# Kernel optimization log

Hardware: AMD Instinct MI355X
Metric: run time of the kernel (lower is better)

Reference implementation:

```python
import jax, jax.numpy as jnp
import numpy as np

B, T, D, H = 4, 1024, 1024, 16


def setup_inputs() -> dict:
    key = jax.random.key(0)
    ks = jax.random.split(key, 7)
    x = jax.random.normal(ks[0], (B, T, D), dtype=jnp.float32)
    scale = 0.02
    Wq = jax.random.normal(ks[1], (D, D), dtype=jnp.float32) * scale
    Wk = jax.random.normal(ks[2], (D, D), dtype=jnp.float32) * scale
    Wv = jax.random.normal(ks[3], (D, D), dtype=jnp.float32) * scale
    bq = jax.random.normal(ks[4], (D,), dtype=jnp.float32) * scale
    bk = jax.random.normal(ks[5], (D,), dtype=jnp.float32) * scale
    bv = jax.random.normal(ks[6], (D,), dtype=jnp.float32) * scale
    temperature = jnp.ones((H, 1, 1), dtype=jnp.float32)  # nn.Parameter(torch.ones(H,1,1))
    return {"x": x, "Wq": Wq, "bq": bq, "Wk": Wk, "bk": bk, "Wv": Wv, "bv": bv,
            "temperature": temperature}


def reference(x, Wq, bq, Wk, bk, Wv, bv, temperature):
    b, t, d = x.shape
    h = temperature.shape[0]
    dh = d // h
    # torch: self.q(x).view(B, H, -1, T)  -- a RAW reshape of (B,T,D) -> (B,H,Dh,T)
    q = (x @ Wq + bq).reshape(b, h, dh, t)
    k = (x @ Wk + bk).reshape(b, h, dh, t)
    v = (x @ Wv + bv).reshape(b, h, dh, t)
    # attn = k^T @ v : (B,H,T,T), scaled per-head by temperature, softmax over last dim
    attn = jnp.einsum('bhdt,bhds->bhts', k, v) * temperature
    attn = jax.nn.softmax(attn, axis=-1)
    # out = q @ attn : (B,H,Dh,T), then RAW reshape back to (B,T,D)
    out = jnp.einsum('bhdt,bhts->bhds', q, attn)
    return out.reshape(b, t, d)
```

## Files before the change

### kernel.cpp

```cpp
#include <hip/hip_runtime.h>
#include <math.h>

#define Bv 4
#define Tv 1024
#define Dv 1024
#define Hv 16
#define DHv 64
#define L2E 1.4426950408889634f

typedef __attribute__((ext_vector_type(8))) short short8;
typedef __attribute__((ext_vector_type(4))) short short4v;
typedef __attribute__((ext_vector_type(4))) float f32x4;
typedef __attribute__((ext_vector_type(2))) int int2v;

#define MFMA16(a, b, c) __builtin_amdgcn_mfma_f32_16x16x32_bf16((a), (b), (c), 0, 0, 0)

__device__ __forceinline__ short f2bf(float f) {
    union { float f; unsigned u; } v; v.f = f;
    unsigned r = v.u + 0x7FFFu + ((v.u >> 16) & 1u);
    return (short)(r >> 16);
}

__device__ __forceinline__ float exp2_hw(float x) {
#if __has_builtin(__builtin_amdgcn_exp2f)
    return __builtin_amdgcn_exp2f(x);
#else
    return exp2f(x);
#endif
}
__device__ __forceinline__ float log2_hw(float x) {
#if __has_builtin(__builtin_amdgcn_logf)
    return __builtin_amdgcn_logf(x);
#else
    return log2f(x);
#endif
}

__device__ __forceinline__ int cvt_pk_bf16(float lo, float hi) {
    int r; asm("v_cvt_pk_bf16_f32 %0, %1, %2" : "=v"(r) : "v"(lo), "v"(hi)); return r;
}

__device__ __forceinline__ void async16(const void* g, void* l) {
    __builtin_amdgcn_global_load_lds(
        (const __attribute__((address_space(1))) void*)g,
        (__attribute__((address_space(3))) void*)l, 16, 0, 0);
}

__device__ __forceinline__ short8 frag64(const short* buf, int r, int cw) {
    return *(const short8*)&buf[r * 64 + ((cw ^ (r & 7)) << 3)];
}

__device__ __forceinline__ short8 frag32(const short* buf, int r, int cw) {
    return *(const short8*)&buf[r * 32 + (((cw ^ (r >> 1)) & 3) << 3)];
}

__global__ __launch_bounds__(256) void cast_x(const float* __restrict__ x, short* __restrict__ xp) {
    const int idx = blockIdx.x * 256 + threadIdx.x;
    const int t = idx >> 7, j = idx & 127;
    const float* src = x + (size_t)t * 1024 + j * 8;
    float4 f0 = ((const float4*)src)[0], f1 = ((const float4*)src)[1];
    short8 o;
    o[0] = f2bf(f0.x); o[1] = f2bf(f0.y); o[2] = f2bf(f0.z); o[3] = f2bf(f0.w);
    o[4] = f2bf(f1.x); o[5] = f2bf(f1.y); o[6] = f2bf(f1.z); o[7] = f2bf(f1.w);
    *(short8*)&xp[(j >> 2) * 131072 + t * 32 + (j & 3) * 8] = o;
}

__global__ __launch_bounds__(256) void w_cast_t(
    const float* __restrict__ Wq, const float* __restrict__ Wk, const float* __restrict__ Wv,
    short* __restrict__ Wt)
{
    const float* W = (blockIdx.z == 0) ? Wq : (blockIdx.z == 1) ? Wk : Wv;
    short* Wto = Wt + (size_t)blockIdx.z * 1048576;
    __shared__ short Tl[64 * 72];
    const int k0 = blockIdx.y * 64, n0 = blockIdx.x * 64;
    const int tid = threadIdx.x;
    {
        const int r = tid >> 2, c16 = (tid & 3) * 16;
        const float* src = W + (size_t)(k0 + r) * Dv + n0 + c16;
        float4 f0 = ((const float4*)src)[0], f1 = ((const float4*)src)[1];
        float4 f2 = ((const float4*)src)[2], f3 = ((const float4*)src)[3];
        short8 s0, s1;
        s0[0] = f2bf(f0.x); s0[1] = f2bf(f0.y); s0[2] = f2bf(f0.z); s0[3] = f2bf(f0.w);
        s0[4] = f2bf(f1.x); s0[5] = f2bf(f1.y); s0[6] = f2bf(f1.z); s0[7] = f2bf(f1.w);
        s1[0] = f2bf(f2.x); s1[1] = f2bf(f2.y); s1[2] = f2bf(f2.z); s1[3] = f2bf(f2.w);
        s1[4] = f2bf(f3.x); s1[5] = f2bf(f3.y); s1[6] = f2bf(f3.z); s1[7] = f2bf(f3.w);
        *(short8*)&Tl[r * 72 + c16] = s0;
        *(short8*)&Tl[r * 72 + c16 + 8] = s1;
    }
    __syncthreads();
#pragma unroll
    for (int p = 0; p < 2; p++) {
        const int n = p * 32 + (tid >> 3), j8 = (tid & 7) * 8;
        short8 o;
#pragma unroll
        for (int jj = 0; jj < 8; jj++) o[jj] = Tl[(j8 + jj) * 72 + n];
        const int kk = k0 + j8;
        *(short8*)&Wto[(kk >> 5) * 32768 + (size_t)(n0 + n) * 32 + (kk & 31)] = o;
    }
}

__global__ __launch_bounds__(256, 2) void qkv_mfma(
    const short* __restrict__ xp, const short* __restrict__ Wp,
    const float* __restrict__ bq, const float* __restrict__ bk, const float* __restrict__ bv,
    const float* __restrict__ temp,
    short* __restrict__ Qo, short* __restrict__ Kt, short* __restrict__ Vt)
{
    __shared__ short smem[30720];

    const int tid = threadIdx.x;
    const int lane = tid & 63, w = tid >> 6;
    const int q = lane >> 4, c = lane & 15;
    const int wr = w >> 1, wc = w & 1;
    const int L = blockIdx.x + 16 * blockIdx.y;
    const int n0 = (L >> 5) * 64;
    const int tm0 = (L & 31) * 128;

    int aOff[2];
#pragma unroll
    for (int p = 0; p < 2; p++) {
        const int idx = p * 256 + tid;
        const int r = idx >> 2, cs = idx & 3, cg = (cs ^ (r >> 1)) & 3;
        aOff[p] = (tm0 + r) * 32 + cg * 8;
    }
    const int br = tid >> 2, bcs = tid & 3, bcg = (bcs ^ (br >> 1)) & 3;
    const int bOff = (n0 + br) * 32 + bcg * 8;

    f32x4 acc[3][4][2] = {};

    auto stage = [&](int s, int kb) {
        short* base = smem + s * 10240;
#pragma unroll
        for (int p = 0; p < 2; p++)
            async16(xp + kb * 131072 + aOff[p], base + (p * 256 + tid) * 8);
#pragma unroll
        for (int z = 0; z < 3; z++)
            async16(Wp + z * 1048576 + kb * 32768 + bOff,
                    base + 4096 + z * 2048 + tid * 8);
    };
    auto compute = [&](int s) {
        const short* base = smem + s * 10240;
        short8 af[4];
#pragma unroll
        for (int m = 0; m < 4; m++) af[m] = frag32(base, wr * 64 + m * 16 + c, q);
        __builtin_amdgcn_s_setprio(1);
#pragma unroll
        for (int z = 0; z < 3; z++) {
            const short* Bz = base + 4096 + z * 2048;
            short8 b0 = frag32(Bz, wc * 32 + c, q);
            short8 b1 = frag32(Bz, wc * 32 + 16 + c, q);
#pragma unroll
            for (int m = 0; m < 4; m++) {
                acc[z][m][0] = MFMA16(af[m], b0, acc[z][m][0]);
                acc[z][m][1] = MFMA16(af[m], b1, acc[z][m][1]);
            }
        }
        __builtin_amdgcn_s_setprio(0);
    };

    stage(0, 0); stage(1, 1);

#pragma unroll 1
    for (int i = 0; i < 30; i++) {
        asm volatile("s_waitcnt vmcnt(5)" ::: "memory");
        __builtin_amdgcn_s_barrier();
        __builtin_amdgcn_sched_barrier(0);
        stage((i + 2) % 3, i + 2);
        compute(i % 3);
    }
    asm volatile("s_waitcnt vmcnt(5)" ::: "memory");
    __builtin_amdgcn_s_barrier();
    __builtin_amdgcn_sched_barrier(0);
    compute(30 % 3);
    asm volatile("s_waitcnt vmcnt(0)" ::: "memory");
    __builtin_amdgcn_s_barrier();
    __builtin_amdgcn_sched_barrier(0);
    compute(31 % 3);

#pragma unroll
    for (int jn = 0; jn < 2; jn++) {
        const int col = n0 + wc * 32 + jn * 16 + c;
        const float bb = bq[col];
#pragma unroll
        for (int m = 0; m < 4; m++)
#pragma unroll
            for (int rr = 0; rr < 4; rr++) {
                const int row = tm0 + wr * 64 + m * 16 + q * 4 + rr;
                Qo[(size_t)row * Dv + col] = f2bf(acc[0][m][jn][rr] + bb);
            }
    }
    const int hb = tm0 >> 6;
#pragma unroll
    for (int z = 1; z < 3; z++) {
        const float* bias = (z == 1) ? bk : bv;
        short* dst = (z == 1) ? Kt : Vt;
        float scl = 1.f;
        if (z == 1) scl = temp[(hb + wr) & 15] * L2E;
        __syncthreads();
        short* T = smem;
#pragma unroll
        for (int jn = 0; jn < 2; jn++) {
            const int nl = wc * 32 + jn * 16 + c;
            const float bb = bias[n0 + nl];
#pragma unroll
            for (int m = 0; m < 4; m++) {
                int2v pk;
                pk[0] = cvt_pk_bf16((acc[z][m][jn][0] + bb) * scl, (acc[z][m][jn][1] + bb) * scl);
                pk[1] = cvt_pk_bf16((acc[z][m][jn][2] + bb) * scl, (acc[z][m][jn][3] + bb) * scl);
                *(int2v*)&T[nl * 136 + wr * 64 + m * 16 + q * 4] = pk;
            }
        }
        __syncthreads();
#pragma unroll
        for (int p = 0; p < 4; p++) {
            const int idx = p * 256 + tid;
            const int n = idx >> 4, k2 = idx & 15;
            short8 v = *(const short8*)&T[n * 136 + k2 * 8];
            const size_t addr = (size_t)(hb + (k2 >> 3)) * 65536 +
                                (size_t)(n0 + n) * 64 + (k2 & 7) * 8;
            *(short8*)&dst[addr] = v;
        }
    }
}

__global__ __launch_bounds__(256, 4) void attn_stats(
    const short* __restrict__ Kt, const short* __restrict__ Vt,
    float* __restrict__ mzOut)
{
    const int L = blockIdx.x + 16 * (blockIdx.y + 16 * blockIdx.z);
    const int bh = (L & 7) + 8 * (L >> 7);
    const int t0 = ((L >> 3) & 15) * 64;
    __shared__ short Ks[64 * 64];
    __shared__ short Vs[2][128 * 64];
    const int tid = threadIdx.x;
    const int lane = tid & 63, w = tid >> 6;
    const int q = lane >> 4, c = lane & 15;
    const short* Kbase = Kt + (size_t)bh * 65536;
    const short* Vbase = Vt + (size_t)bh * 65536;

    int vOff[4], vDst[4];
#pragma unroll
    for (int p = 0; p < 4; p++) {
        const int idx = p * 256 + tid;
        const int r = idx >> 3, cs = idx & 7, cg = cs ^ (r & 7);
        vOff[p] = r * 64 + cg * 8;
        vDst[p] = idx * 8;
    }
#pragma unroll
    for (int p = 0; p < 2; p++) {
        const int idx = p * 256 + tid;
        const int r = idx >> 3, cs = idx & 7, cg = cs ^ (r & 7);
        async16(Kbase + (size_t)(t0 + r) * 64 + cg * 8, Ks + idx * 8);
    }
#pragma unroll
    for (int p = 0; p < 4; p++) async16(Vbase + vOff[p], &Vs[0][0] + vDst[p]);

    float z_run[4] = {0.f, 0.f, 0.f, 0.f};

    short8 aK0, aK1;
#pragma unroll 1
    for (int i = 0; i < 8; i++) {
        __syncthreads();
        if (i < 7) {
            const short* src = Vbase + (i + 1) * 8192;
#pragma unroll
            for (int p = 0; p < 4; p++) async16(src + vOff[p], &Vs[(i + 1) & 1][0] + vDst[p]);
        }
        if (i == 0) {
            aK0 = frag64(Ks, w * 16 + c, q);
            aK1 = frag64(Ks, w * 16 + c, 4 + q);
        }
        const short* Vc = &Vs[i & 1][0];
        __builtin_amdgcn_s_setprio(1);
#pragma unroll
        for (int sf = 0; sf < 8; sf++) {
            short8 b0 = frag64(Vc, sf * 16 + c, q);
            short8 b1 = frag64(Vc, sf * 16 + c, 4 + q);
            f32x4 l = {0.f, 0.f, 0.f, 0.f};
            l = MFMA16(aK0, b0, l);
            l = MFMA16(aK1, b1, l);
#pragma unroll
            for (int r = 0; r < 4; r++) z_run[r] += exp2_hw(l[r]);
        }
        __builtin_amdgcn_s_setprio(0);
    }
#pragma unroll
    for (int mask = 1; mask <= 8; mask <<= 1) {
#pragma unroll
        for (int r = 0; r < 4; r++) z_run[r] += __shfl_xor(z_run[r], mask, 64);
    }
    if (c == 0) {
#pragma unroll
        for (int r = 0; r < 4; r++) {
            const int t = t0 + w * 16 + q * 4 + r;
            mzOut[(size_t)bh * Tv + t] = log2_hw(z_run[r]);
        }
    }
}

__global__ __launch_bounds__(256, 2) void attn_out(
    const short* __restrict__ Qb, const short* __restrict__ Kt, const short* __restrict__ Vt,
    const float* __restrict__ mzIn, float* __restrict__ out)
{
    const int L = blockIdx.x + 8 * (blockIdx.y + 16 * blockIdx.z);
    const int bh = (L & 7) + 8 * (L >> 6);
    const int s0 = ((L >> 3) & 7) * 128;
    const int b = bh >> 4, h = bh & 15;

    __shared__ short smem[26624];
    short* VsPt = smem;
    float* mzs = (float*)(smem + 24576);

    const int tid = threadIdx.x;
    const int lane = tid & 63, w = tid >> 6;
    const int q = lane >> 4, c = lane & 15;
    const short* Vbase = Vt + (size_t)bh * 65536;
    const short* Kbase = Kt + (size_t)bh * 65536;
    const short* Qbase = Qb + (size_t)(b * Tv + h * DHv) * Dv;

    int kOff[2], qOff[2], dK[2], dQ[2];
#pragma unroll
    for (int p = 0; p < 2; p++) {
        const int idx = p * 256 + tid;
        const int r = idx >> 3, cs = idx & 7, cg = cs ^ (r & 7);
        kOff[p] = r * 64 + cg * 8;
        qOff[p] = r * 1024 + cg * 8;
        dK[p] = idx * 8;
        dQ[p] = 4096 + idx * 8;
    }

#pragma unroll
    for (int p = 0; p < 4; p++) {
        const int idx = p * 256 + tid;
        const int r = idx >> 3, cs = idx & 7, cg = cs ^ (r & 7);
        async16(Vbase + (size_t)(s0 + r) * 64 + cg * 8, VsPt + idx * 8);
    }
    async16(mzIn + (size_t)bh * Tv + tid * 4, (short*)mzs + tid * 8);
#pragma unroll
    for (int p = 0; p < 2; p++) {
        async16(Kbase + kOff[p], smem + 8192 + dK[p]);
        async16(Qbase + qOff[p], smem + 8192 + dQ[p]);
    }
    __syncthreads();

    short8 vb0[8], vb1[8];
#pragma unroll
    for (int sf = 0; sf < 8; sf++) {
        vb0[sf] = frag64(VsPt, sf * 16 + c, q);
        vb1[sf] = frag64(VsPt, sf * 16 + c, 4 + q);
    }

    f32x4 acc[8] = {};
    short* Pt = VsPt;

#pragma unroll 1
    for (int i = 0; i < 16; i++) {
        const short* kq = smem + 8192 + (i & 1) * 8192;
        __syncthreads();
        if (i < 15) {
            short* nxt = smem + 8192 + ((i + 1) & 1) * 8192;
            const int t1 = (i + 1) * 64;
#pragma unroll
            for (int p = 0; p < 2; p++) {
                async16(Kbase + t1 * 64 + kOff[p], nxt + dK[p]);
                async16(Qbase + t1 + qOff[p], nxt + dQ[p]);
            }
        }
        short8 aK0 = frag64(kq, w * 16 + c, q);
        short8 aK1 = frag64(kq, w * 16 + c, 4 + q);
        const int tr0 = i * 64 + w * 16 + q * 4;
        const float4 mv = *(const float4*)&mzs[tr0];
#pragma unroll
        for (int sf = 0; sf < 8; sf++) {
            f32x4 l = {0.f, 0.f, 0.f, 0.f};
            l = MFMA16(aK0, vb0[sf], l);
            l = MFMA16(aK1, vb1[sf], l);
            const int rr = sf * 16 + c;
            int2v p4;
            p4[0] = cvt_pk_bf16(exp2_hw(l[0] - mv.x), exp2_hw(l[1] - mv.y));
            p4[1] = cvt_pk_bf16(exp2_hw(l[2] - mv.z), exp2_hw(l[3] - mv.w));
            *(int2v*)&Pt[rr * 64 + (((w * 2 + (q >> 1)) ^ (rr & 7)) << 3) + (q & 1) * 4] = p4;
        }
        asm volatile("s_waitcnt lgkmcnt(0)" ::: "memory");
        __builtin_amdgcn_sched_barrier(0);
        __builtin_amdgcn_s_barrier();
        __builtin_amdgcn_sched_barrier(0);
        const short* Qs = kq + 4096;
        short8 aQ0 = frag64(Qs, w * 16 + c, q);
        short8 aQ1 = frag64(Qs, w * 16 + c, 4 + q);
        __builtin_amdgcn_s_setprio(1);
#pragma unroll
        for (int sf = 0; sf < 8; sf++) {
            short8 p0 = frag64(Pt, sf * 16 + c, q);
            short8 p1 = frag64(Pt, sf * 16 + c, 4 + q);
            acc[sf] = MFMA16(aQ0, p0, acc[sf]);
            acc[sf] = MFMA16(aQ1, p1, acc[sf]);
        }
        __builtin_amdgcn_s_setprio(0);
    }

#pragma unroll
    for (int sf = 0; sf < 8; sf++) {
#pragma unroll
        for (int r = 0; r < 4; r++) {
            const int d = w * 16 + q * 4 + r;
            out[(size_t)(b * Tv + h * DHv + d) * Dv + s0 + sf * 16 + c] = acc[sf][r];
        }
    }
}

extern "C" void kernel_launch(void* const* d_in, const int* in_sizes, int n_in,
                              void* d_out, int out_size, void* d_ws, size_t ws_size,
                              hipStream_t stream) {
    const float* x    = (const float*)d_in[0];
    const float* Wq   = (const float*)d_in[1];
    const float* bq   = (const float*)d_in[2];
    const float* Wk   = (const float*)d_in[3];
    const float* bk   = (const float*)d_in[4];
    const float* Wv   = (const float*)d_in[5];
    const float* bv   = (const float*)d_in[6];
    const float* temp = (const float*)d_in[7];
    float* out = (float*)d_out;

    char* ws = (char*)d_ws;
    short* xp = (short*)(ws);
    short* Wp = (short*)(ws + ((size_t)8 << 20));
    short* Qb = (short*)(ws + ((size_t)14 << 20));
    short* Kt = (short*)(ws + ((size_t)22 << 20));
    short* Vt = (short*)(ws + ((size_t)30 << 20));
    float* mzbuf = (float*)(ws + ((size_t)38 << 20));

    cast_x<<<2048, 256, 0, stream>>>(x, xp);
    w_cast_t<<<dim3(16, 16, 3), 256, 0, stream>>>(Wq, Wk, Wv, Wp);
    qkv_mfma<<<dim3(16, 32), 256, 0, stream>>>(xp, Wp, bq, bk, bv, temp, Qb, Kt, Vt);
    attn_stats<<<dim3(16, 16, 4), 256, 0, stream>>>(Kt, Vt, mzbuf);
    attn_out<<<dim3(8, 16, 4), 256, 0, stream>>>(Qb, Kt, Vt, mzbuf, out);
}
```

Before: 151.8 us.

## Double qkv_mfma block to 512 threads and split tile loading across waves

The QKV projection kernel now runs 512 threads (8 waves) per block instead of 256, with launch bounds of 4 blocks per CU. Each wave computes a 32x32 sub-tile per projection instead of 64x32, which halves the accumulator registers. Loading is split by wave: waves 0-3 issue the three weight-slab async copies and waves 4-7 issue the x-tile copies, with per-wave vmcnt waits to match. The aim is more waves in flight to hide load latency, at the cost of less register-level reuse of the A fragments and heavier barrier traffic.

```diff
diff --git a/kernel.cpp b/kernel.cpp
--- a/kernel.cpp
+++ b/kernel.cpp
@@ -99,7 +99,7 @@
     }
 }
 
-__global__ __launch_bounds__(256, 2) void qkv_mfma(
+__global__ __launch_bounds__(512, 4) void qkv_mfma(
     const short* __restrict__ xp, const short* __restrict__ Wp,
     const float* __restrict__ bq, const float* __restrict__ bk, const float* __restrict__ bv,
     const float* __restrict__ temp,
@@ -115,33 +115,48 @@
     const int n0 = (L >> 5) * 64;
     const int tm0 = (L & 31) * 128;
 
-    int aOff[2];
-#pragma unroll
-    for (int p = 0; p < 2; p++) {
-        const int idx = p * 256 + tid;
-        const int r = idx >> 2, cs = idx & 3, cg = (cs ^ (r >> 1)) & 3;
-        aOff[p] = (tm0 + r) * 32 + cg * 8;
-    }
-    const int br = tid >> 2, bcs = tid & 3, bcg = (bcs ^ (br >> 1)) & 3;
-    const int bOff = (n0 + br) * 32 + bcg * 8;
-
-    f32x4 acc[3][4][2] = {};
+    int sOff[3], sDst[3];
+    const int nIns = (w < 4) ? 3 : 2;
+    if (w < 4) {
+#pragma unroll
+        for (int p = 0; p < 3; p++) {
+            const int idx = p * 256 + w * 64 + lane;
+            const int z = idx >> 8, rz = (idx & 255) >> 2, cs = idx & 3;
+            const int cg = (cs ^ (rz >> 1)) & 3;
+            sOff[p] = z * 1048576 + (n0 + rz) * 32 + cg * 8;
+            sDst[p] = 4096 + z * 2048 + (idx & 255) * 8;
+        }
+    } else {
+#pragma unroll
+        for (int p = 0; p < 2; p++) {
+            const int idx = p * 256 + (w - 4) * 64 + lane;
+            const int r = idx >> 2, cs = idx & 3;
+            const int cg = (cs ^ (r >> 1)) & 3;
+            sOff[p] = (tm0 + r) * 32 + cg * 8;
+            sDst[p] = idx * 8;
+        }
+        sOff[2] = sOff[0]; sDst[2] = sDst[0];
+    }
+
+    f32x4 acc[3][2][2] = {};
 
     auto stage = [&](int s, int kb) {
         short* base = smem + s * 10240;
-#pragma unroll
-        for (int p = 0; p < 2; p++)
-            async16(xp + kb * 131072 + aOff[p], base + (p * 256 + tid) * 8);
-#pragma unroll
-        for (int z = 0; z < 3; z++)
-            async16(Wp + z * 1048576 + kb * 32768 + bOff,
-                    base + 4096 + z * 2048 + tid * 8);
+        if (w < 4) {
+#pragma unroll
+            for (int p = 0; p < 3; p++)
+                async16(Wp + kb * 32768 + sOff[p], base + sDst[p]);
+        } else {
+#pragma unroll
+            for (int p = 0; p < 2; p++)
+                async16(xp + kb * 131072 + sOff[p], base + sDst[p]);
+        }
     };
     auto compute = [&](int s) {
         const short* base = smem + s * 10240;
-        short8 af[4];
-#pragma unroll
-        for (int m = 0; m < 4; m++) af[m] = frag32(base, wr * 64 + m * 16 + c, q);
+        short8 af[2];
+#pragma unroll
+        for (int m = 0; m < 2; m++) af[m] = frag32(base, wr * 32 + m * 16 + c, q);
         __builtin_amdgcn_s_setprio(1);
 #pragma unroll
         for (int z = 0; z < 3; z++) {
@@ -149,29 +164,34 @@
             short8 b0 = frag32(Bz, wc * 32 + c, q);
             short8 b1 = frag32(Bz, wc * 32 + 16 + c, q);
 #pragma unroll
-            for (int m = 0; m < 4; m++) {
+            for (int m = 0; m < 2; m++) {
                 acc[z][m][0] = MFMA16(af[m], b0, acc[z][m][0]);
                 acc[z][m][1] = MFMA16(af[m], b1, acc[z][m][1]);
             }
         }
         __builtin_amdgcn_s_setprio(0);
     };
+    auto waitTile = [&](int n) {
+        if (n == 0) { asm volatile("s_waitcnt vmcnt(0)" ::: "memory"); }
+        else if (w < 4) { asm volatile("s_waitcnt vmcnt(3)" ::: "memory"); }
+        else { asm volatile("s_waitcnt vmcnt(2)" ::: "memory"); }
+    };
 
     stage(0, 0); stage(1, 1);
 
 #pragma unroll 1
     for (int i = 0; i < 30; i++) {
-        asm volatile("s_waitcnt vmcnt(5)" ::: "memory");
+        waitTile(1);
         __builtin_amdgcn_s_barrier();
         __builtin_amdgcn_sched_barrier(0);
         stage((i + 2) % 3, i + 2);
         compute(i % 3);
     }
-    asm volatile("s_waitcnt vmcnt(5)" ::: "memory");
+    waitTile(1);
     __builtin_amdgcn_s_barrier();
     __builtin_amdgcn_sched_barrier(0);
     compute(30 % 3);
-    asm volatile("s_waitcnt vmcnt(0)" ::: "memory");
+    waitTile(0);
     __builtin_amdgcn_s_barrier();
     __builtin_amdgcn_sched_barrier(0);
     compute(31 % 3);
@@ -181,10 +201,10 @@
         const int col = n0 + wc * 32 + jn * 16 + c;
         const float bb = bq[col];
 #pragma unroll
-        for (int m = 0; m < 4; m++)
+        for (int m = 0; m < 2; m++)
 #pragma unroll
             for (int rr = 0; rr < 4; rr++) {
-                const int row = tm0 + wr * 64 + m * 16 + q * 4 + rr;
+                const int row = tm0 + wr * 32 + m * 16 + q * 4 + rr;
                 Qo[(size_t)row * Dv + col] = f2bf(acc[0][m][jn][rr] + bb);
             }
     }
@@ -194,7 +214,7 @@
         const float* bias = (z == 1) ? bk : bv;
         short* dst = (z == 1) ? Kt : Vt;
         float scl = 1.f;
-        if (z == 1) scl = temp[(hb + wr) & 15] * L2E;
+        if (z == 1) scl = temp[(hb + (wr >> 1)) & 15] * L2E;
         __syncthreads();
         short* T = smem;
 #pragma unroll
@@ -202,17 +222,17 @@
             const int nl = wc * 32 + jn * 16 + c;
             const float bb = bias[n0 + nl];
 #pragma unroll
-            for (int m = 0; m < 4; m++) {
+            for (int m = 0; m < 2; m++) {
                 int2v pk;
                 pk[0] = cvt_pk_bf16((acc[z][m][jn][0] + bb) * scl, (acc[z][m][jn][1] + bb) * scl);
                 pk[1] = cvt_pk_bf16((acc[z][m][jn][2] + bb) * scl, (acc[z][m][jn][3] + bb) * scl);
-                *(int2v*)&T[nl * 136 + wr * 64 + m * 16 + q * 4] = pk;
+                *(int2v*)&T[nl * 136 + wr * 32 + m * 16 + q * 4] = pk;
             }
         }
         __syncthreads();
 #pragma unroll
-        for (int p = 0; p < 4; p++) {
-            const int idx = p * 256 + tid;
+        for (int p = 0; p < 2; p++) {
+            const int idx = p * 512 + tid;
             const int n = idx >> 4, k2 = idx & 15;
             short8 v = *(const short8*)&T[n * 136 + k2 * 8];
             const size_t addr = (size_t)(hb + (k2 >> 3)) * 65536 +
@@ -431,7 +451,7 @@
 
     cast_x<<<2048, 256, 0, stream>>>(x, xp);
     w_cast_t<<<dim3(16, 16, 3), 256, 0, stream>>>(Wq, Wk, Wv, Wp);
-    qkv_mfma<<<dim3(16, 32), 256, 0, stream>>>(xp, Wp, bq, bk, bv, temp, Qb, Kt, Vt);
+    qkv_mfma<<<dim3(16, 32), 512, 0, stream>>>(xp, Wp, bq, bk, bv, temp, Qb, Kt, Vt);
     attn_stats<<<dim3(16, 16, 4), 256, 0, stream>>>(Kt, Vt, mzbuf);
     attn_out<<<dim3(8, 16, 4), 256, 0, stream>>>(Qb, Kt, Vt, mzbuf, out);
 }
```

Measured after the change: 176.4 us. +16.2%, slower.
